# Kernel optimization log

Hardware: AMD Instinct MI355X
Metric: run time of the kernel (lower is better)

The kernel has to match this reference:

```python
import jax, jax.numpy as jnp
import numpy as np

ALPHA = 1.0
BLOCK = 128  # row block size for the pairwise L1 reduction


def _pairwise_score(features, a):
    # score[i, j] = sum_k |f[i,k] - f[j,k]| * a[k]
    # computed in row blocks to avoid the O(n^2*d) broadcast intermediate
    n, d = features.shape
    av = a[:, 0]  # [d]
    fb = features.reshape(n // BLOCK, BLOCK, d)

    def blk(fblk):  # fblk: [B, d]
        diff = jnp.abs(fblk[:, None, :] - features[None, :, :])  # [B, n, d]
        return jnp.einsum('bnd,d->bn', diff, av)                  # [B, n]

    return jax.lax.map(blk, fb).reshape(n, n)


def setup_inputs() -> dict:
    key = jax.random.key(0)
    n, d = 8192, 256
    features = jax.random.normal(key, (n, d), dtype=jnp.float32)
    a = jnp.full((d, 1), 0.01, dtype=jnp.float32)  # nn.init.constant_(a, 0.01)
    return {"features": features, "a": a}


def reference(features, a):
    score = _pairwise_score(features, a)                 # [n, n]
    adjacency = jnp.exp(-ALPHA * jax.nn.relu(score))     # [n, n]
    # D^{-1/2} A D^{-1/2} via row/col elementwise scaling (== diag mm mm)
    dsq = jnp.sum(adjacency, axis=1) ** -0.5             # [n]
    normalized = dsq[:, None] * adjacency * dsq[None, :]
    return (normalized, adjacency)
```

## Files before the change

kernel.cpp:

```cpp
#include <hip/hip_runtime.h>
#include <math.h>

typedef unsigned int uint;
typedef float f32x4 __attribute__((ext_vector_type(4)));

__device__ __forceinline__ uint fenc(float f) {
    uint u = __float_as_uint(f);
    return (u & 0x80000000u) ? ~u : (u | 0x80000000u);
}
__device__ __forceinline__ float fdec(uint u) {
    uint v = (u & 0x80000000u) ? (u & 0x7FFFFFFFu) : ~u;
    return __uint_as_float(v);
}

__device__ __forceinline__ void ntst(float* p, float a, float b, float c, float d) {
    f32x4 t; t.x = a; t.y = b; t.z = c; t.w = d;
    __builtin_nontemporal_store(t, (f32x4*)p);
}
__device__ __forceinline__ void cst(float* p, float a, float b, float c, float d) {
    f32x4 t; t.x = a; t.y = b; t.z = c; t.w = d;
    *(f32x4*)p = t;
}

__global__ __launch_bounds__(256) void init_kernel(uint* __restrict__ flags,
                                                   const float* __restrict__ A,
                                                   int d)
{
    const int t = threadIdx.x;
    if (t == 0) { flags[0] = 0u; flags[1] = 0xFFFFFFFFu; flags[2] = 0u; }
    __syncthreads();
    for (int k = t; k < d; k += 256)
        if (A[k] < 0.f) atomicOr(&flags[0], 1u);
}

__global__ __launch_bounds__(256) void minmax_kernel(const float* __restrict__ F,
                                                     const float* __restrict__ A,
                                                     uint* __restrict__ flags,
                                                     int n, int d)
{
    const int total4 = n * d / 4;
    float lmin = 3.4e38f, lmax = -3.4e38f;
    for (int e4 = blockIdx.x * 256 + threadIdx.x; e4 < total4; e4 += gridDim.x * 256) {
        int e = e4 * 4;
        int dk = e % d;
        float4 f = *(const float4*)(F + e);
        float4 a = *(const float4*)(A + dk);
        float g0 = fabsf(a.x) * f.x, g1 = fabsf(a.y) * f.y;
        float g2 = fabsf(a.z) * f.z, g3 = fabsf(a.w) * f.w;
        lmin = fminf(lmin, fminf(fminf(g0, g1), fminf(g2, g3)));
        lmax = fmaxf(lmax, fmaxf(fmaxf(g0, g1), fmaxf(g2, g3)));
    }
    #pragma unroll
    for (int m = 1; m < 64; m <<= 1) {
        lmin = fminf(lmin, __shfl_xor(lmin, m));
        lmax = fmaxf(lmax, __shfl_xor(lmax, m));
    }
    if ((threadIdx.x & 63) == 0) {
        atomicMin(&flags[1], fenc(lmin));
        atomicMax(&flags[2], fenc(lmax));
    }
}

__global__ __launch_bounds__(256) void quant_kernel(const float* __restrict__ F,
                                                    const float* __restrict__ A,
                                                    const uint* __restrict__ flags,
                                                    uint* __restrict__ Q,
                                                    float* __restrict__ rowsum,
                                                    int n, int d)
{
    const int t = threadIdx.x;
    const int r = blockIdx.x * 32 + (t & 31);
    if (t < 32) rowsum[blockIdx.x * 32 + t] = 0.f;
    const int kqb = t >> 5;
    const int d4 = d >> 2;
    const float gmin = fdec(flags[1]), gmax = fdec(flags[2]);
    const float span = gmax - gmin;
    const float inv = span > 0.f ? 255.f / span : 0.f;
    for (int kq = kqb; kq < d4; kq += 8) {
        float4 f = *(const float4*)(F + (size_t)r * d + kq * 4);
        float4 a = *(const float4*)(A + kq * 4);
        uint q0 = 0, q1 = 0, q2 = 0, q3 = 0;
        if (a.x > 0.f) q0 = (uint)fminf(fmaxf((a.x * f.x - gmin) * inv + 0.5f, 0.f), 255.f);
        if (a.y > 0.f) q1 = (uint)fminf(fmaxf((a.y * f.y - gmin) * inv + 0.5f, 0.f), 255.f);
        if (a.z > 0.f) q2 = (uint)fminf(fmaxf((a.z * f.z - gmin) * inv + 0.5f, 0.f), 255.f);
        if (a.w > 0.f) q3 = (uint)fminf(fmaxf((a.w * f.w - gmin) * inv + 0.5f, 0.f), 255.f);
        Q[(size_t)kq * n + r] = q0 | (q1 << 8) | (q2 << 16) | (q3 << 24);
    }
}

__device__ __forceinline__ void sad_core(const uint* __restrict__ Q, int n, int chunks,
                                         int i0, int j0, int t,
                                         uint (&acc)[8][8],
                                         uint (&As)[16][128], uint (&Bs)[16][128])
{
    const int tx = t & 15, ty = t >> 4;
    const int kk0 = t >> 5;
    const int col = 4 * (t & 31);

    uint4 sa[2], sb[2];
    #pragma unroll
    for (int j = 0; j < 2; ++j) {
        size_t g = ((size_t)(kk0 + 8 * j)) * n;
        sa[j] = *(const uint4*)(Q + g + i0 + col);
        sb[j] = *(const uint4*)(Q + g + j0 + col);
    }

    for (int c = 0; c < chunks; ++c) {
        ((uint4*)&As[0][0])[t]       = sa[0];
        ((uint4*)&As[0][0])[256 + t] = sa[1];
        ((uint4*)&Bs[0][0])[t]       = sb[0];
        ((uint4*)&Bs[0][0])[256 + t] = sb[1];
        __syncthreads();

        if (c + 1 < chunks) {
            #pragma unroll
            for (int j = 0; j < 2; ++j) {
                size_t g = ((size_t)((c + 1) * 16 + kk0 + 8 * j)) * n;
                sa[j] = *(const uint4*)(Q + g + i0 + col);
                sb[j] = *(const uint4*)(Q + g + j0 + col);
            }
        }

        #pragma unroll
        for (int kk = 0; kk < 16; ++kk) {
            uint ar[8], br[8];
            *(uint4*)&ar[0] = *(const uint4*)&As[kk][4 * ty];
            *(uint4*)&ar[4] = *(const uint4*)&As[kk][64 + 4 * ty];
            *(uint4*)&br[0] = *(const uint4*)&Bs[kk][4 * tx];
            *(uint4*)&br[4] = *(const uint4*)&Bs[kk][64 + 4 * tx];
            #pragma unroll
            for (int m = 0; m < 8; ++m)
                #pragma unroll
                for (int cc = 0; cc < 8; ++cc)
                    acc[m][cc] = __builtin_amdgcn_sad_u8(ar[m], br[cc], acc[m][cc]);
        }
        __syncthreads();
    }
}

__device__ __forceinline__ void tri_decode(int b, int& bx, int& by) {
    bx = (int)((sqrtf(8.f * (float)b + 1.f) - 1.f) * 0.5f);
    while ((bx + 1) * (bx + 2) / 2 <= b) ++bx;
    while (bx * (bx + 1) / 2 > b) --bx;
    by = b - bx * (bx + 1) / 2;
}

__global__ __launch_bounds__(256, 3) void pass1_sad(const uint* __restrict__ Q,
                                                    const uint* __restrict__ flags,
                                                    float* __restrict__ adj,
                                                    float* __restrict__ rowsum,
                                                    int n, int d)
{
    if (flags[0] != 0u) return;

    __shared__ uint As[16][128];
    __shared__ uint Bs[16][128];

    int bx, by; tri_decode(blockIdx.x, bx, by);
    const int t = threadIdx.x, tx = t & 15, ty = t >> 4;
    const int i0 = by * 128, j0 = bx * 128;
    const bool diag = (bx == by);

    const float gmin = fdec(flags[1]), gmax = fdec(flags[2]);
    const float nstep = (gmin - gmax) * (1.f / 255.f);

    uint acc[8][8] = {};
    sad_core(Q, n, (d >> 2) >> 4, i0, j0, t, acc, As, Bs);

    #pragma unroll
    for (int m = 0; m < 8; ++m)
        #pragma unroll
        for (int cc = 0; cc < 8; ++cc)
            acc[m][cc] = __float_as_uint(__expf(nstep * (float)acc[m][cc]));

    #pragma unroll
    for (int m = 0; m < 8; ++m) {
        const int row = i0 + (m >> 2) * 64 + 4 * ty + (m & 3);
        #pragma unroll
        for (int qh = 0; qh < 2; ++qh)
            cst(adj + (size_t)row * n + j0 + qh * 64 + 4 * tx,
                __uint_as_float(acc[m][qh * 4 + 0]),
                __uint_as_float(acc[m][qh * 4 + 1]),
                __uint_as_float(acc[m][qh * 4 + 2]),
                __uint_as_float(acc[m][qh * 4 + 3]));
    }

    if (!diag) {
        #pragma unroll
        for (int h = 0; h < 2; ++h)
            #pragma unroll
            for (int qh = 0; qh < 2; ++qh)
                #pragma unroll
                for (int cc = 0; cc < 4; ++cc) {
                    const int r = j0 + qh * 64 + 4 * tx + cc;
                    cst(adj + (size_t)r * n + i0 + 64 * h + 4 * ty,
                        __uint_as_float(acc[4 * h + 0][qh * 4 + cc]),
                        __uint_as_float(acc[4 * h + 1][qh * 4 + cc]),
                        __uint_as_float(acc[4 * h + 2][qh * 4 + cc]),
                        __uint_as_float(acc[4 * h + 3][qh * 4 + cc]));
                }
    }

    #pragma unroll
    for (int m = 0; m < 8; ++m) {
        const int row = i0 + (m >> 2) * 64 + 4 * ty + (m & 3);
        float rs = 0.f;
        #pragma unroll
        for (int cc = 0; cc < 8; ++cc) rs += __uint_as_float(acc[m][cc]);
        rs += __shfl_xor(rs, 1);
        rs += __shfl_xor(rs, 2);
        rs += __shfl_xor(rs, 4);
        rs += __shfl_xor(rs, 8);
        if (tx == 0) atomicAdd(rowsum + row, rs);
    }

    if (!diag) {
        float cs[8];
        #pragma unroll
        for (int cc = 0; cc < 8; ++cc) {
            float s = 0.f;
            #pragma unroll
            for (int m = 0; m < 8; ++m) s += __uint_as_float(acc[m][cc]);
            s += __shfl_xor(s, 16);
            s += __shfl_xor(s, 32);
            cs[cc] = s;
        }
        if ((t & 48) == 0) {
            #pragma unroll
            for (int qh = 0; qh < 2; ++qh)
                #pragma unroll
                for (int cc = 0; cc < 4; ++cc)
                    atomicAdd(rowsum + j0 + qh * 64 + 4 * tx + cc, cs[qh * 4 + cc]);
        }
    }
}

__global__ __launch_bounds__(256) void adj_fp32_kernel(
    const float* __restrict__ F, const float* __restrict__ A,
    const uint* __restrict__ flags,
    float* __restrict__ adj, float* __restrict__ rowsum, int n, int d)
{
    if (flags[0] == 0u) return;

    __shared__ __align__(16) float As[32][132];
    __shared__ __align__(16) float Bs[32][132];
    __shared__ float aw[256];

    const int t  = threadIdx.x;
    const int tx = t & 15;
    const int ty = t >> 4;
    const int nb = n / 128;

    for (int k = t; k < d; k += 256) aw[k] = A[k];

    for (int bt = blockIdx.x; bt < nb * nb; bt += gridDim.x) {
        const int i0 = (bt / nb) * 128;
        const int j0 = (bt % nb) * 128;

        float acc[2][2][4][4] = {};
        const int lr = t >> 3;
        const int lk = (t & 7) << 2;

        for (int kc = 0; kc < d; kc += 32) {
            __syncthreads();
            #pragma unroll
            for (int s = 0; s < 4; ++s) {
                int r = lr + 32 * s;
                float4 v = *(const float4*)(F + (size_t)(i0 + r) * d + kc + lk);
                As[lk + 0][r] = v.x; As[lk + 1][r] = v.y;
                As[lk + 2][r] = v.z; As[lk + 3][r] = v.w;
                float4 u = *(const float4*)(F + (size_t)(j0 + r) * d + kc + lk);
                Bs[lk + 0][r] = u.x; Bs[lk + 1][r] = u.y;
                Bs[lk + 2][r] = u.z; Bs[lk + 3][r] = u.w;
            }
            __syncthreads();

            #pragma unroll
            for (int k = 0; k < 32; ++k) {
                float av[2][4], bv[2][4];
                *(float4*)&av[0][0] = *(const float4*)&As[k][4 * ty];
                *(float4*)&av[1][0] = *(const float4*)&As[k][64 + 4 * ty];
                *(float4*)&bv[0][0] = *(const float4*)&Bs[k][4 * tx];
                *(float4*)&bv[1][0] = *(const float4*)&Bs[k][64 + 4 * tx];
                const float w = aw[kc + k];
                #pragma unroll
                for (int p = 0; p < 2; ++p)
                    #pragma unroll
                    for (int m = 0; m < 4; ++m)
                        #pragma unroll
                        for (int q = 0; q < 2; ++q)
                            #pragma unroll
                            for (int c = 0; c < 4; ++c)
                                acc[p][q][m][c] += fabsf(av[p][m] - bv[q][c]) * w;
            }
        }

        #pragma unroll
        for (int p = 0; p < 2; ++p) {
            #pragma unroll
            for (int m = 0; m < 4; ++m) {
                const int row = i0 + p * 64 + ty * 4 + m;
                float rs = 0.f;
                #pragma unroll
                for (int q = 0; q < 2; ++q) {
                    float4 v;
                    v.x = __expf(-fmaxf(acc[p][q][m][0], 0.f));
                    v.y = __expf(-fmaxf(acc[p][q][m][1], 0.f));
                    v.z = __expf(-fmaxf(acc[p][q][m][2], 0.f));
                    v.w = __expf(-fmaxf(acc[p][q][m][3], 0.f));
                    rs += (v.x + v.y) + (v.z + v.w);
                    *(float4*)(adj + (size_t)row * n + j0 + q * 64 + tx * 4) = v;
                }
                rs += __shfl_xor(rs, 1);
                rs += __shfl_xor(rs, 2);
                rs += __shfl_xor(rs, 4);
                rs += __shfl_xor(rs, 8);
                if (tx == 0) atomicAdd(rowsum + row, rs);
            }
        }
        __syncthreads();
    }
}

__global__ __launch_bounds__(256) void dsq_kernel(
    const float* __restrict__ rowsum, float* __restrict__ dsq, int n)
{
    int i = blockIdx.x * 256 + threadIdx.x;
    if (i < n) dsq[i] = 1.f / sqrtf(rowsum[i]);
}

__global__ __launch_bounds__(256) void norm_kernel(
    const float* __restrict__ adj, const float* __restrict__ dsq,
    float* __restrict__ out, int n)
{
    const int i = blockIdx.y;
    const float di = dsq[i];
    const int j0 = blockIdx.x * 4096 + threadIdx.x * 4;
    #pragma unroll
    for (int k = 0; k < 4; ++k) {
        const int j = j0 + k * 1024;
        if (j >= n) return;
        f32x4 a = __builtin_nontemporal_load((const f32x4*)(adj + (size_t)i * n + j));
        float4 dj = *(const float4*)(dsq + j);
        ntst(out + (size_t)i * n + j,
             di * a.x * dj.x, di * a.y * dj.y, di * a.z * dj.z, di * a.w * dj.w);
    }
}

extern "C" void kernel_launch(void* const* d_in, const int* in_sizes, int n_in,
                              void* d_out, int out_size, void* d_ws, size_t ws_size,
                              hipStream_t stream)
{
    const float* F = (const float*)d_in[0];
    const float* A = (const float*)d_in[1];
    const int d = in_sizes[1];
    const int n = in_sizes[0] / d;

    float* nrm    = (float*)d_out;
    float* adj    = nrm + (size_t)n * n;
    uint*  flags  = (uint*)d_ws;
    float* rowsum = (float*)d_ws + 8;
    float* dsq    = rowsum + n;
    uint* Q = (uint*)d_out;

    init_kernel<<<dim3(1), dim3(256), 0, stream>>>(flags, A, d);
    minmax_kernel<<<dim3(256), dim3(256), 0, stream>>>(F, A, flags, n, d);
    quant_kernel<<<dim3(n / 32), dim3(256), 0, stream>>>(F, A, flags, Q, rowsum, n, d);

    const int nb = n / 128;
    const int tri = nb * (nb + 1) / 2;
    pass1_sad<<<dim3(tri), dim3(256), 0, stream>>>(Q, flags, adj, rowsum, n, d);
    adj_fp32_kernel<<<dim3(1024), dim3(256), 0, stream>>>(F, A, flags, adj, rowsum, n, d);

    dsq_kernel<<<dim3((n + 255) / 256), dim3(256), 0, stream>>>(rowsum, dsq, n);

    dim3 gridN((n + 4095) / 4096, n);
    norm_kernel<<<gridN, dim3(256), 0, stream>>>(adj, dsq, nrm, n);
}
```

Before: 298.8 us.

## Store 16-bit SAD scores, fuse exp and normalization into tiled symmetric pass

```diff
diff --git a/kernel.cpp b/kernel.cpp
--- a/kernel.cpp
+++ b/kernel.cpp
@@ -2,6 +2,7 @@
 #include <math.h>
 
 typedef unsigned int uint;
+typedef unsigned short ushort_t;
 typedef float f32x4 __attribute__((ext_vector_type(4)));
 
 __device__ __forceinline__ uint fenc(float f) {
@@ -145,11 +146,164 @@
     by = b - bx * (bx + 1) / 2;
 }
 
-__global__ __launch_bounds__(256, 3) void pass1_sad(const uint* __restrict__ Q,
-                                                    const uint* __restrict__ flags,
-                                                    float* __restrict__ adj,
-                                                    float* __restrict__ rowsum,
-                                                    int n, int d)
+__global__ __launch_bounds__(256, 3) void pass1_sad16(const uint* __restrict__ Q,
+                                                      const uint* __restrict__ flags,
+                                                      ushort_t* s16,
+                                                      float* __restrict__ rowsum,
+                                                      int n, int d)
+{
+    if (flags[0] != 0u) return;
+
+    __shared__ uint As[16][128];
+    __shared__ uint Bs[16][128];
+
+    int bx, by; tri_decode(blockIdx.x, bx, by);
+    const int t = threadIdx.x, tx = t & 15, ty = t >> 4;
+    const int i0 = by * 128, j0 = bx * 128;
+    const bool diag = (bx == by);
+
+    const float gmin = fdec(flags[1]), gmax = fdec(flags[2]);
+    const float nstep = (gmin - gmax) * (1.f / 255.f);
+
+    uint acc[8][8] = {};
+    sad_core(Q, n, (d >> 2) >> 4, i0, j0, t, acc, As, Bs);
+
+    #pragma unroll
+    for (int m = 0; m < 8; ++m) {
+        const int row = i0 + (m >> 2) * 64 + 4 * ty + (m & 3);
+        const size_t rb = ((size_t)row * n + j0) * 2;
+        #pragma unroll
+        for (int qh = 0; qh < 2; ++qh) {
+            uint2 v;
+            v.x = (acc[m][qh * 4 + 0] & 0xFFFFu) | (acc[m][qh * 4 + 1] << 16);
+            v.y = (acc[m][qh * 4 + 2] & 0xFFFFu) | (acc[m][qh * 4 + 3] << 16);
+            *(uint2*)(s16 + rb + qh * 64 + 4 * tx) = v;
+        }
+    }
+
+    float cs[8] = {0.f, 0.f, 0.f, 0.f, 0.f, 0.f, 0.f, 0.f};
+    #pragma unroll
+    for (int m = 0; m < 8; ++m) {
+        const int row = i0 + (m >> 2) * 64 + 4 * ty + (m & 3);
+        float rs = 0.f;
+        #pragma unroll
+        for (int cc = 0; cc < 8; ++cc) {
+            float e = __expf(nstep * (float)acc[m][cc]);
+            rs += e; cs[cc] += e;
+        }
+        rs += __shfl_xor(rs, 1);
+        rs += __shfl_xor(rs, 2);
+        rs += __shfl_xor(rs, 4);
+        rs += __shfl_xor(rs, 8);
+        if (tx == 0) atomicAdd(rowsum + row, rs);
+    }
+    if (!diag) {
+        #pragma unroll
+        for (int cc = 0; cc < 8; ++cc) {
+            float s = cs[cc];
+            s += __shfl_xor(s, 16);
+            s += __shfl_xor(s, 32);
+            cs[cc] = s;
+        }
+        if ((t & 48) == 0) {
+            #pragma unroll
+            for (int qh = 0; qh < 2; ++qh)
+                #pragma unroll
+                for (int cc = 0; cc < 4; ++cc)
+                    atomicAdd(rowsum + j0 + qh * 64 + 4 * tx + cc, cs[qh * 4 + cc]);
+        }
+    }
+}
+
+__global__ __launch_bounds__(256) void norm_tiled(const ushort_t* s16,
+                                                  const uint* __restrict__ flags,
+                                                  const float* __restrict__ rowsum,
+                                                  float* __restrict__ adj,
+                                                  float* nrm, int n)
+{
+    if (flags[0] != 0u) return;
+
+    int bx, by; tri_decode(blockIdx.x, bx, by);
+    const int t = threadIdx.x, tx = t & 15, ty = t >> 4;
+    const int i0 = by * 128, j0 = bx * 128;
+    const bool diag = (bx == by);
+
+    const float gmin = fdec(flags[1]), gmax = fdec(flags[2]);
+    const float nstep = (gmin - gmax) * (1.f / 255.f);
+
+    float e[8][8];
+    #pragma unroll
+    for (int m = 0; m < 8; ++m) {
+        const int row = i0 + (m >> 2) * 64 + 4 * ty + (m & 3);
+        const size_t rb = ((size_t)row * n + j0) * 2;
+        #pragma unroll
+        for (int qh = 0; qh < 2; ++qh) {
+            uint2 v = *(const uint2*)(s16 + rb + qh * 64 + 4 * tx);
+            e[m][qh * 4 + 0] = __expf(nstep * (float)(v.x & 0xFFFFu));
+            e[m][qh * 4 + 1] = __expf(nstep * (float)(v.x >> 16));
+            e[m][qh * 4 + 2] = __expf(nstep * (float)(v.y & 0xFFFFu));
+            e[m][qh * 4 + 3] = __expf(nstep * (float)(v.y >> 16));
+        }
+    }
+
+    float dr[8], dc[8];
+    #pragma unroll
+    for (int m = 0; m < 8; ++m)
+        dr[m] = rsqrtf(rowsum[i0 + (m >> 2) * 64 + 4 * ty + (m & 3)]);
+    {
+        float4 c0 = *(const float4*)(rowsum + j0 + 4 * tx);
+        float4 c1 = *(const float4*)(rowsum + j0 + 64 + 4 * tx);
+        dc[0] = rsqrtf(c0.x); dc[1] = rsqrtf(c0.y);
+        dc[2] = rsqrtf(c0.z); dc[3] = rsqrtf(c0.w);
+        dc[4] = rsqrtf(c1.x); dc[5] = rsqrtf(c1.y);
+        dc[6] = rsqrtf(c1.z); dc[7] = rsqrtf(c1.w);
+    }
+
+    __syncthreads();
+
+    #pragma unroll
+    for (int m = 0; m < 8; ++m) {
+        const int row = i0 + (m >> 2) * 64 + 4 * ty + (m & 3);
+        const float dm = dr[m];
+        #pragma unroll
+        for (int qh = 0; qh < 2; ++qh) {
+            float* ap = adj + (size_t)row * n + j0 + qh * 64 + 4 * tx;
+            float* np = nrm + (size_t)row * n + j0 + qh * 64 + 4 * tx;
+            ntst(ap, e[m][qh * 4 + 0], e[m][qh * 4 + 1],
+                     e[m][qh * 4 + 2], e[m][qh * 4 + 3]);
+            ntst(np, e[m][qh * 4 + 0] * dm * dc[qh * 4 + 0],
+                     e[m][qh * 4 + 1] * dm * dc[qh * 4 + 1],
+                     e[m][qh * 4 + 2] * dm * dc[qh * 4 + 2],
+                     e[m][qh * 4 + 3] * dm * dc[qh * 4 + 3]);
+        }
+    }
+
+    if (!diag) {
+        #pragma unroll
+        for (int h = 0; h < 2; ++h)
+            #pragma unroll
+            for (int qh = 0; qh < 2; ++qh)
+                #pragma unroll
+                for (int cc = 0; cc < 4; ++cc) {
+                    const int r = j0 + qh * 64 + 4 * tx + cc;
+                    const float dcv = dc[qh * 4 + cc];
+                    float* ap = adj + (size_t)r * n + i0 + 64 * h + 4 * ty;
+                    float* np = nrm + (size_t)r * n + i0 + 64 * h + 4 * ty;
+                    ntst(ap, e[4 * h + 0][qh * 4 + cc], e[4 * h + 1][qh * 4 + cc],
+                             e[4 * h + 2][qh * 4 + cc], e[4 * h + 3][qh * 4 + cc]);
+                    ntst(np, e[4 * h + 0][qh * 4 + cc] * dr[4 * h + 0] * dcv,
+                             e[4 * h + 1][qh * 4 + cc] * dr[4 * h + 1] * dcv,
+                             e[4 * h + 2][qh * 4 + cc] * dr[4 * h + 2] * dcv,
+                             e[4 * h + 3][qh * 4 + cc] * dr[4 * h + 3] * dcv);
+                }
+    }
+}
+
+__global__ __launch_bounds__(256, 3) void pass1_sadW(const uint* __restrict__ Q,
+                                                     const uint* __restrict__ flags,
+                                                     float* __restrict__ adj,
+                                                     float* __restrict__ rowsum,
+                                                     int n, int d)
 {
     if (flags[0] != 0u) return;
 
@@ -184,7 +338,6 @@
                 __uint_as_float(acc[m][qh * 4 + 2]),
                 __uint_as_float(acc[m][qh * 4 + 3]));
     }
-
     if (!diag) {
         #pragma unroll
         for (int h = 0; h < 2; ++h)
@@ -213,7 +366,6 @@
         rs += __shfl_xor(rs, 8);
         if (tx == 0) atomicAdd(rowsum + row, rs);
     }
-
     if (!diag) {
         float cs[8];
         #pragma unroll
@@ -322,28 +474,23 @@
     }
 }
 
-__global__ __launch_bounds__(256) void dsq_kernel(
-    const float* __restrict__ rowsum, float* __restrict__ dsq, int n)
-{
-    int i = blockIdx.x * 256 + threadIdx.x;
-    if (i < n) dsq[i] = 1.f / sqrtf(rowsum[i]);
-}
-
-__global__ __launch_bounds__(256) void norm_kernel(
-    const float* __restrict__ adj, const float* __restrict__ dsq,
-    float* __restrict__ out, int n)
-{
+__global__ __launch_bounds__(256) void norm_linear(
+    const float* __restrict__ adj, const float* __restrict__ rowsum,
+    const uint* __restrict__ flags, float* __restrict__ out, int n, int onlyNeg)
+{
+    if (onlyNeg && flags[0] == 0u) return;
     const int i = blockIdx.y;
-    const float di = dsq[i];
+    const float di = rsqrtf(rowsum[i]);
     const int j0 = blockIdx.x * 4096 + threadIdx.x * 4;
     #pragma unroll
     for (int k = 0; k < 4; ++k) {
         const int j = j0 + k * 1024;
         if (j >= n) return;
         f32x4 a = __builtin_nontemporal_load((const f32x4*)(adj + (size_t)i * n + j));
-        float4 dj = *(const float4*)(dsq + j);
+        float4 rj = *(const float4*)(rowsum + j);
         ntst(out + (size_t)i * n + j,
-             di * a.x * dj.x, di * a.y * dj.y, di * a.z * dj.z, di * a.w * dj.w);
+             di * a.x * rsqrtf(rj.x), di * a.y * rsqrtf(rj.y),
+             di * a.z * rsqrtf(rj.z), di * a.w * rsqrtf(rj.w));
     }
 }
 
@@ -360,8 +507,11 @@
     float* adj    = nrm + (size_t)n * n;
     uint*  flags  = (uint*)d_ws;
     float* rowsum = (float*)d_ws + 8;
-    float* dsq    = rowsum + n;
-    uint* Q = (uint*)d_out;
+
+    const size_t wsHead = (((size_t)(8 + n) * 4) + 255) & ~(size_t)255;
+    const size_t need = wsHead + (size_t)n * d;
+    const bool big = (ws_size >= need);
+    uint* Q = big ? (uint*)((char*)d_ws + wsHead) : (uint*)d_out;
 
     init_kernel<<<dim3(1), dim3(256), 0, stream>>>(flags, A, d);
     minmax_kernel<<<dim3(256), dim3(256), 0, stream>>>(F, A, flags, n, d);
@@ -369,11 +519,18 @@
 
     const int nb = n / 128;
     const int tri = nb * (nb + 1) / 2;
-    pass1_sad<<<dim3(tri), dim3(256), 0, stream>>>(Q, flags, adj, rowsum, n, d);
-    adj_fp32_kernel<<<dim3(1024), dim3(256), 0, stream>>>(F, A, flags, adj, rowsum, n, d);
-
-    dsq_kernel<<<dim3((n + 255) / 256), dim3(256), 0, stream>>>(rowsum, dsq, n);
-
-    dim3 gridN((n + 4095) / 4096, n);
-    norm_kernel<<<gridN, dim3(256), 0, stream>>>(adj, dsq, nrm, n);
-}
+    dim3 gridL((n + 4095) / 4096, n);
+
+    if (big) {
+        pass1_sad16<<<dim3(tri), dim3(256), 0, stream>>>(Q, flags, (ushort_t*)nrm,
+                                                         rowsum, n, d);
+        adj_fp32_kernel<<<dim3(1024), dim3(256), 0, stream>>>(F, A, flags, adj, rowsum, n, d);
+        norm_tiled<<<dim3(tri), dim3(256), 0, stream>>>((const ushort_t*)nrm, flags,
+                                                        rowsum, adj, nrm, n);
+        norm_linear<<<gridL, dim3(256), 0, stream>>>(adj, rowsum, flags, nrm, n, 1);
+    } else {
+        pass1_sadW<<<dim3(tri), dim3(256), 0, stream>>>(Q, flags, adj, rowsum, n, d);
+        adj_fp32_kernel<<<dim3(1024), dim3(256), 0, stream>>>(F, A, flags, adj, rowsum, n, d);
+        norm_linear<<<gridL, dim3(256), 0, stream>>>(adj, rowsum, flags, nrm, n, 0);
+    }
+}
```

Result: slower. 317.4 us (+6.2%).

## Split triangular pass into SAD pass and fused mirror+normalize pass

Applied to the files above, without the earlier changes.

```diff
diff --git a/kernel.cpp b/kernel.cpp
--- a/kernel.cpp
+++ b/kernel.cpp
@@ -156,33 +156,121 @@
     __shared__ uint As[16][128];
     __shared__ uint Bs[16][128];
 
+    const int t = threadIdx.x, tx = t & 15, ty = t >> 4;
+    const float gmin = fdec(flags[1]), gmax = fdec(flags[2]);
+    const float nstep = (gmin - gmax) * (1.f / 255.f);
+
+    #pragma unroll 1
+    for (int tt = 0; tt < 2; ++tt) {
+        const int b = blockIdx.x * 2 + tt;
+        int bx, by; tri_decode(b, bx, by);
+        const int i0 = by * 128, j0 = bx * 128;
+        const bool diag = (bx == by);
+
+        uint acc[8][8] = {};
+        sad_core(Q, n, (d >> 2) >> 4, i0, j0, t, acc, As, Bs);
+
+        #pragma unroll
+        for (int m = 0; m < 8; ++m)
+            #pragma unroll
+            for (int cc = 0; cc < 8; ++cc)
+                acc[m][cc] = __float_as_uint(__expf(nstep * (float)acc[m][cc]));
+
+        #pragma unroll
+        for (int m = 0; m < 8; ++m) {
+            const int row = i0 + (m >> 2) * 64 + 4 * ty + (m & 3);
+            #pragma unroll
+            for (int qh = 0; qh < 2; ++qh)
+                cst(adj + (size_t)row * n + j0 + qh * 64 + 4 * tx,
+                    __uint_as_float(acc[m][qh * 4 + 0]),
+                    __uint_as_float(acc[m][qh * 4 + 1]),
+                    __uint_as_float(acc[m][qh * 4 + 2]),
+                    __uint_as_float(acc[m][qh * 4 + 3]));
+        }
+
+        #pragma unroll
+        for (int m = 0; m < 8; ++m) {
+            const int row = i0 + (m >> 2) * 64 + 4 * ty + (m & 3);
+            float rs = 0.f;
+            #pragma unroll
+            for (int cc = 0; cc < 8; ++cc) rs += __uint_as_float(acc[m][cc]);
+            rs += __shfl_xor(rs, 1);
+            rs += __shfl_xor(rs, 2);
+            rs += __shfl_xor(rs, 4);
+            rs += __shfl_xor(rs, 8);
+            if (tx == 0) atomicAdd(rowsum + row, rs);
+        }
+        if (!diag) {
+            float cs[8];
+            #pragma unroll
+            for (int cc = 0; cc < 8; ++cc) {
+                float s = 0.f;
+                #pragma unroll
+                for (int m = 0; m < 8; ++m) s += __uint_as_float(acc[m][cc]);
+                s += __shfl_xor(s, 16);
+                s += __shfl_xor(s, 32);
+                cs[cc] = s;
+            }
+            if ((t & 48) == 0) {
+                #pragma unroll
+                for (int qh = 0; qh < 2; ++qh)
+                    #pragma unroll
+                    for (int cc = 0; cc < 4; ++cc)
+                        atomicAdd(rowsum + j0 + qh * 64 + 4 * tx + cc, cs[qh * 4 + cc]);
+            }
+        }
+    }
+}
+
+__global__ __launch_bounds__(256) void pass2_norm(const float* __restrict__ adj_r,
+                                                  float* __restrict__ adj,
+                                                  const float* __restrict__ rowsum,
+                                                  const uint* __restrict__ flags,
+                                                  float* __restrict__ nrm, int n)
+{
+    if (flags[0] != 0u) return;
+
     int bx, by; tri_decode(blockIdx.x, bx, by);
     const int t = threadIdx.x, tx = t & 15, ty = t >> 4;
     const int i0 = by * 128, j0 = bx * 128;
     const bool diag = (bx == by);
 
-    const float gmin = fdec(flags[1]), gmax = fdec(flags[2]);
-    const float nstep = (gmin - gmax) * (1.f / 255.f);
-
-    uint acc[8][8] = {};
-    sad_core(Q, n, (d >> 2) >> 4, i0, j0, t, acc, As, Bs);
-
-    #pragma unroll
-    for (int m = 0; m < 8; ++m)
-        #pragma unroll
-        for (int cc = 0; cc < 8; ++cc)
-            acc[m][cc] = __float_as_uint(__expf(nstep * (float)acc[m][cc]));
-
+    float e[8][8];
     #pragma unroll
     for (int m = 0; m < 8; ++m) {
         const int row = i0 + (m >> 2) * 64 + 4 * ty + (m & 3);
         #pragma unroll
+        for (int qh = 0; qh < 2; ++qh) {
+            float4 v = *(const float4*)(adj_r + (size_t)row * n + j0 + qh * 64 + 4 * tx);
+            e[m][qh * 4 + 0] = v.x; e[m][qh * 4 + 1] = v.y;
+            e[m][qh * 4 + 2] = v.z; e[m][qh * 4 + 3] = v.w;
+        }
+    }
+
+    float dr[8], dc[8];
+    #pragma unroll
+    for (int m = 0; m < 8; ++m)
+        dr[m] = rsqrtf(rowsum[i0 + (m >> 2) * 64 + 4 * ty + (m & 3)]);
+    {
+        float4 c0 = *(const float4*)(rowsum + j0 + 4 * tx);
+        float4 c1 = *(const float4*)(rowsum + j0 + 64 + 4 * tx);
+        dc[0] = rsqrtf(c0.x); dc[1] = rsqrtf(c0.y);
+        dc[2] = rsqrtf(c0.z); dc[3] = rsqrtf(c0.w);
+        dc[4] = rsqrtf(c1.x); dc[5] = rsqrtf(c1.y);
+        dc[6] = rsqrtf(c1.z); dc[7] = rsqrtf(c1.w);
+    }
+
+    #pragma unroll
+    for (int m = 0; m < 8; ++m) {
+        const int row = i0 + (m >> 2) * 64 + 4 * ty + (m & 3);
+        const float dm = dr[m];
+        #pragma unroll
         for (int qh = 0; qh < 2; ++qh)
-            cst(adj + (size_t)row * n + j0 + qh * 64 + 4 * tx,
-                __uint_as_float(acc[m][qh * 4 + 0]),
-                __uint_as_float(acc[m][qh * 4 + 1]),
-                __uint_as_float(acc[m][qh * 4 + 2]),
-                __uint_as_float(acc[m][qh * 4 + 3]));
+            ntst(nrm + (size_t)row * n + j0 + qh * 64 + 4 * tx,
+                 e[m][qh * 4 + 0] * dm * dc[qh * 4 + 0],
+                 e[m][qh * 4 + 1] * dm * dc[qh * 4 + 1],
+                 e[m][qh * 4 + 2] * dm * dc[qh * 4 + 2],
+                 e[m][qh * 4 + 3] * dm * dc[qh * 4 + 3]);
     }
 
     if (!diag) {
@@ -193,45 +281,16 @@
                 #pragma unroll
                 for (int cc = 0; cc < 4; ++cc) {
                     const int r = j0 + qh * 64 + 4 * tx + cc;
-                    cst(adj + (size_t)r * n + i0 + 64 * h + 4 * ty,
-                        __uint_as_float(acc[4 * h + 0][qh * 4 + cc]),
-                        __uint_as_float(acc[4 * h + 1][qh * 4 + cc]),
-                        __uint_as_float(acc[4 * h + 2][qh * 4 + cc]),
-                        __uint_as_float(acc[4 * h + 3][qh * 4 + cc]));
+                    const float dcv = dc[qh * 4 + cc];
+                    float* ap = adj + (size_t)r * n + i0 + 64 * h + 4 * ty;
+                    float* np = nrm + (size_t)r * n + i0 + 64 * h + 4 * ty;
+                    ntst(ap, e[4 * h + 0][qh * 4 + cc], e[4 * h + 1][qh * 4 + cc],
+                             e[4 * h + 2][qh * 4 + cc], e[4 * h + 3][qh * 4 + cc]);
+                    ntst(np, e[4 * h + 0][qh * 4 + cc] * dr[4 * h + 0] * dcv,
+                             e[4 * h + 1][qh * 4 + cc] * dr[4 * h + 1] * dcv,
+                             e[4 * h + 2][qh * 4 + cc] * dr[4 * h + 2] * dcv,
+                             e[4 * h + 3][qh * 4 + cc] * dr[4 * h + 3] * dcv);
                 }
-    }
-
-    #pragma unroll
-    for (int m = 0; m < 8; ++m) {
-        const int row = i0 + (m >> 2) * 64 + 4 * ty + (m & 3);
-        float rs = 0.f;
-        #pragma unroll
-        for (int cc = 0; cc < 8; ++cc) rs += __uint_as_float(acc[m][cc]);
-        rs += __shfl_xor(rs, 1);
-        rs += __shfl_xor(rs, 2);
-        rs += __shfl_xor(rs, 4);
-        rs += __shfl_xor(rs, 8);
-        if (tx == 0) atomicAdd(rowsum + row, rs);
-    }
-
-    if (!diag) {
-        float cs[8];
-        #pragma unroll
-        for (int cc = 0; cc < 8; ++cc) {
-            float s = 0.f;
-            #pragma unroll
-            for (int m = 0; m < 8; ++m) s += __uint_as_float(acc[m][cc]);
-            s += __shfl_xor(s, 16);
-            s += __shfl_xor(s, 32);
-            cs[cc] = s;
-        }
-        if ((t & 48) == 0) {
-            #pragma unroll
-            for (int qh = 0; qh < 2; ++qh)
-                #pragma unroll
-                for (int cc = 0; cc < 4; ++cc)
-                    atomicAdd(rowsum + j0 + qh * 64 + 4 * tx + cc, cs[qh * 4 + cc]);
-        }
     }
 }
 
@@ -322,28 +381,23 @@
     }
 }
 
-__global__ __launch_bounds__(256) void dsq_kernel(
-    const float* __restrict__ rowsum, float* __restrict__ dsq, int n)
-{
-    int i = blockIdx.x * 256 + threadIdx.x;
-    if (i < n) dsq[i] = 1.f / sqrtf(rowsum[i]);
-}
-
-__global__ __launch_bounds__(256) void norm_kernel(
-    const float* __restrict__ adj, const float* __restrict__ dsq,
-    float* __restrict__ out, int n)
-{
+__global__ __launch_bounds__(256) void norm_linear(
+    const float* __restrict__ adj, const float* __restrict__ rowsum,
+    const uint* __restrict__ flags, float* __restrict__ out, int n)
+{
+    if (flags[0] == 0u) return;
     const int i = blockIdx.y;
-    const float di = dsq[i];
+    const float di = rsqrtf(rowsum[i]);
     const int j0 = blockIdx.x * 4096 + threadIdx.x * 4;
     #pragma unroll
     for (int k = 0; k < 4; ++k) {
         const int j = j0 + k * 1024;
         if (j >= n) return;
         f32x4 a = __builtin_nontemporal_load((const f32x4*)(adj + (size_t)i * n + j));
-        float4 dj = *(const float4*)(dsq + j);
+        float4 rj = *(const float4*)(rowsum + j);
         ntst(out + (size_t)i * n + j,
-             di * a.x * dj.x, di * a.y * dj.y, di * a.z * dj.z, di * a.w * dj.w);
+             di * a.x * rsqrtf(rj.x), di * a.y * rsqrtf(rj.y),
+             di * a.z * rsqrtf(rj.z), di * a.w * rsqrtf(rj.w));
     }
 }
 
@@ -360,7 +414,6 @@
     float* adj    = nrm + (size_t)n * n;
     uint*  flags  = (uint*)d_ws;
     float* rowsum = (float*)d_ws + 8;
-    float* dsq    = rowsum + n;
     uint* Q = (uint*)d_out;
 
     init_kernel<<<dim3(1), dim3(256), 0, stream>>>(flags, A, d);
@@ -369,11 +422,10 @@
 
     const int nb = n / 128;
     const int tri = nb * (nb + 1) / 2;
-    pass1_sad<<<dim3(tri), dim3(256), 0, stream>>>(Q, flags, adj, rowsum, n, d);
+    pass1_sad<<<dim3(tri / 2), dim3(256), 0, stream>>>(Q, flags, adj, rowsum, n, d);
     adj_fp32_kernel<<<dim3(1024), dim3(256), 0, stream>>>(F, A, flags, adj, rowsum, n, d);
 
-    dsq_kernel<<<dim3((n + 255) / 256), dim3(256), 0, stream>>>(rowsum, dsq, n);
-
-    dim3 gridN((n + 4095) / 4096, n);
-    norm_kernel<<<gridN, dim3(256), 0, stream>>>(adj, dsq, nrm, n);
-}
+    pass2_norm<<<dim3(tri), dim3(256), 0, stream>>>(adj, adj, rowsum, flags, nrm, n);
+    dim3 gridL((n + 4095) / 4096, n);
+    norm_linear<<<gridL, dim3(256), 0, stream>>>(adj, rowsum, flags, nrm, n);
+}
```

Result: no change. 294.9 us, median of 2 (-1.3%).
